# Performance work log

Hardware: AMD Instinct MI355X
Metric: run time of the kernel (lower is better)

The kernel has to match this reference:

```python
import jax, jax.numpy as jnp
import numpy as np

B, C, H, W = 4, 256, 64, 64
R, KH, KW = 4, 3, 3
K = KH * KW  # 9 kernel taps


def _conv2d(x, w, b):
    # plain 3x3 conv, stride 1, pad 1, NCHW
    y = jax.lax.conv_general_dilated(x, w, (1, 1), ((1, 1), (1, 1)),
                                     dimension_numbers=('NCHW', 'OIHW', 'NCHW'))
    return y + b[None, :, None, None]


def _bilinear_sample(x, py, px):
    # x: [B,C,H,W]; py,px: [B,K,H,W] float coords; zero padding outside the image.
    B_, C_, H_, W_ = x.shape
    xf = x.reshape(B_, C_, H_ * W_)
    y0 = jnp.floor(py)
    x0 = jnp.floor(px)
    wy = py - y0
    wx = px - x0
    y0i = y0.astype(jnp.int32)
    x0i = x0.astype(jnp.int32)

    def corner(yi, xi, wgt):
        valid = (yi >= 0) & (yi < H_) & (xi >= 0) & (xi < W_)
        idx = (jnp.clip(yi, 0, H_ - 1) * W_ + jnp.clip(xi, 0, W_ - 1)).reshape(B_, -1)
        vals = jax.vmap(lambda xb, ib: jnp.take(xb, ib, axis=1))(xf, idx)  # [B,C,K*H*W]
        vals = vals.reshape(B_, C_, K, H_, W_)
        w_ = (wgt * valid).astype(x.dtype)[:, None]  # [B,1,K,H,W]
        return vals * w_

    out = corner(y0i, x0i, (1 - wy) * (1 - wx))
    out = out + corner(y0i, x0i + 1, (1 - wy) * wx)
    out = out + corner(y0i + 1, x0i, wy * (1 - wx))
    out = out + corner(y0i + 1, x0i + 1, wy * wx)
    return out  # [B,C,K,H,W]


def _deform_conv(x, offset, weight):
    # DCNv1: offset [B, 2K, H, W], interleaved (dy, dx) per kernel tap.
    B_, C_, H_, W_ = x.shape
    off = offset.reshape(B_, K, 2, H_, W_)
    ky, kx = jnp.meshgrid(jnp.arange(KH), jnp.arange(KW), indexing='ij')
    base_y = (ky.reshape(K) - (KH - 1) // 2).astype(x.dtype)
    base_x = (kx.reshape(K) - (KW - 1) // 2).astype(x.dtype)
    py = (jnp.arange(H_, dtype=x.dtype)[None, None, :, None]
          + base_y[None, :, None, None] + off[:, :, 0])
    px = (jnp.arange(W_, dtype=x.dtype)[None, None, None, :]
          + base_x[None, :, None, None] + off[:, :, 1])
    sampled = _bilinear_sample(x, py, px)  # [B,C,K,H,W]
    wr = weight.reshape(weight.shape[0], C_, K)
    return jnp.einsum('bckhw,ock->bohw', sampled, wr)


def setup_inputs() -> dict:
    key = jax.random.key(0)
    k1, k2, k3 = jax.random.split(key, 3)
    x = jax.random.normal(k1, (B, C, H, W), jnp.float32)
    off_w = jax.random.normal(k2, (R, 2 * K, C, KH, KW), jnp.float32) * 0.01
    off_b = jnp.zeros((R, 2 * K), jnp.float32)
    w = jax.random.normal(k3, (R, C, C, KH, KW), jnp.float32) * (1.0 / np.sqrt(C * K))
    return {"x": x, "off_w": off_w, "off_b": off_b, "w": w}


def reference(x, off_w, off_b, w):
    for r in range(R):  # fixed small layer count
        offset = _conv2d(x, off_w[r], off_b[r])
        x = jax.nn.relu(_deform_conv(x, offset, w[r]))
    return x
```

## Files before the change

### kernel.cpp

```cpp
#include <hip/hip_runtime.h>


#define HW 4096

typedef __attribute__((ext_vector_type(8))) __bf16 bf16x8;
typedef __attribute__((ext_vector_type(4))) float f32x4;
typedef __attribute__((ext_vector_type(8))) unsigned short u16x8;

__device__ inline unsigned int f2bf_bits(float f) {
  unsigned int u = __float_as_uint(f);
  return (u + 0x7fffu + ((u >> 16) & 1u)) >> 16;
}
__device__ inline float bf_hi_f(unsigned short h) {
  return __uint_as_float(((unsigned int)h) << 16);
}

__global__ __launch_bounds__(256) void wpack_kernel(
    const float* __restrict__ w, unsigned short* __restrict__ wph) {
  const int f = blockIdx.x * 256 + threadIdx.x;
  const int j  = f & 7;
  const int l  = (f >> 3) & 63;
  const int nt = (f >> 9) & 15;
  const int q  = (f >> 13) % 72;
  const int r  = f / 589824;
  const int n  = nt * 16 + (l & 15);
  const int kk = q * 32 + ((l >> 4) << 3) + j;
  const int c  = kk & 255, k = kk >> 8;
  wph[f] = (unsigned short)f2bf_bits(w[((r * 256 + n) * 256 + c) * 9 + k]);
}

__global__ __launch_bounds__(256) void offwpack_kernel(
    const float* __restrict__ offw, unsigned short* __restrict__ owph) {
  const int f = blockIdx.x * 256 + threadIdx.x;
  const int j  = f & 7;
  const int l  = (f >> 3) & 63;
  const int nt = (f >> 9) & 1;
  const int q  = (f >> 10) % 72;
  const int r  = f / 73728;
  const int n  = nt * 16 + (l & 15);
  const int kk = q * 32 + ((l >> 4) << 3) + j;
  const int c  = kk & 255, k = kk >> 8;
  const float v = (n < 18) ? offw[((r * 18 + n) * 256 + c) * 9 + k] : 0.f;
  owph[f] = (unsigned short)f2bf_bits(v);
}

__global__ __launch_bounds__(256) void xpose_kernel(
    const float* __restrict__ x, unsigned short* __restrict__ xh) {
  const int p0 = blockIdx.x * 64;
  const int c0 = blockIdx.y * 64;
  const int b  = blockIdx.z;
  __shared__ float sT[64][65];
  const int t = threadIdx.x;
  const int pj = t & 63, ci0 = (t >> 6) * 16;
  const float* __restrict__ xb = x + ((size_t)(b * 256 + c0)) * HW + p0;
#pragma unroll
  for (int u = 0; u < 16; ++u)
    sT[ci0 + u][pj] = xb[(size_t)(ci0 + u) * HW + pj];
  __syncthreads();
  const int pr = t >> 2, cs = (t & 3) * 16;
  u16x8 va, vb;
#pragma unroll
  for (int u = 0; u < 8; ++u) va[u] = (unsigned short)f2bf_bits(sT[cs + u][pr]);
#pragma unroll
  for (int u = 0; u < 8; ++u) vb[u] = (unsigned short)f2bf_bits(sT[cs + 8 + u][pr]);
  const size_t o = ((size_t)b * HW + p0 + pr) * 256 + c0 + cs;
  *(u16x8*)(xh + o) = va;
  *(u16x8*)(xh + o + 8) = vb;
}

__global__ __launch_bounds__(256) void offconv_mfma(
    const unsigned short* __restrict__ xh,
    const unsigned short* __restrict__ owh,
    const float* __restrict__ bias, float* __restrict__ offs) {
  const int gid = blockIdx.x;
  const int b = (gid & 7) >> 1;
  const int idx = ((gid >> 3) << 1) | (gid & 1);
  const int h = idx >> 1, w0 = (idx & 1) << 5;
  const int t = threadIdx.x, lane = t & 63, wv = t >> 6;
  const int frow = lane & 15, fgrp = lane >> 4;
  const int mt = wv & 1, nt = wv >> 1;
  const int m = w0 + mt * 16 + frow;

  f32x4 acc = {0.f, 0.f, 0.f, 0.f};
  const u16x8 z8 = {};
  const size_t xb = (size_t)b * HW;

  for (int k = 0; k < 9; ++k) {
    const int ky = k / 3 - 1, kx = k % 3 - 1;
    if ((unsigned)(h + ky) >= 64u) continue;
    const bool vpx = (unsigned)(m + kx) < 64u;
    const int cpx = (m + kx) < 0 ? 0 : ((m + kx) > 63 ? 63 : (m + kx));
    const size_t abase = (xb + (size_t)((h + ky) * 64 + cpx)) * 256 + fgrp * 8;
#pragma unroll
    for (int cc = 0; cc < 8; ++cc) {
      const int q = k * 8 + cc;
      u16x8 ahr = *(const u16x8*)(xh + abase + cc * 32);
      if (!vpx) ahr = z8;
      const u16x8 bhr = ((const u16x8*)owh)[(q * 2 + nt) * 64 + lane];
      const bf16x8 ah = __builtin_bit_cast(bf16x8, ahr);
      const bf16x8 bh = __builtin_bit_cast(bf16x8, bhr);
      acc = __builtin_amdgcn_mfma_f32_16x16x32_bf16(ah, bh, acc, 0, 0, 0);
    }
  }
  const int oc = nt * 16 + frow;
  if (oc < 18) {
    const float bv = bias[oc];
    const int wbase = w0 + mt * 16 + fgrp * 4;
    float* __restrict__ op = offs + (size_t)(b * 18 + oc) * HW + h * 64 + wbase;
#pragma unroll
    for (int r = 0; r < 4; ++r) op[r] = acc[r] + bv;
  }
}

__global__ __launch_bounds__(512, 4) void deform_mfma(
    const unsigned short* __restrict__ xh,
    const float* __restrict__ offs,
    const unsigned short* __restrict__ wph,
    unsigned short* __restrict__ yth,
    float* __restrict__ outf) {
  const int gid = blockIdx.x;
  const int b = (gid & 7) >> 1;
  const int idx = ((gid >> 3) << 1) | (gid & 1);
  const int h = idx >> 1, w0 = (idx & 1) << 5;
  const int t = threadIdx.x, lane = t & 63, wv = t >> 6;
  const int frow = lane & 15, quad = lane >> 4;
  const int sm = t >> 4, cg = t & 15;

  __shared__ __align__(16) unsigned char smem[19456];
  float* s_cw = (float*)smem;
  int*   s_ci = (int*)(smem + 4608);
  unsigned char* sAb = smem + 9216;

  for (int i = t; i < 288; i += 512) {
    const int k = i >> 5, m = i & 31;
    const int ky = k / 3 - 1, kx = k % 3 - 1;
    const int mw = w0 + m;
    const int pos = h * 64 + mw;
    const float dy = offs[(b * 18 + 2 * k) * HW + pos];
    const float dx = offs[(b * 18 + 2 * k + 1) * HW + pos];
    const float py = (float)(h + ky) + dy;
    const float px = (float)(mw + kx) + dx;
    const float y0f = floorf(py), x0f = floorf(px);
    const float wy = py - y0f, wx = px - x0f;
    const int y0 = (int)y0f, x0 = (int)x0f;
#pragma unroll
    for (int j = 0; j < 4; ++j) {
      const int yi = y0 + (j >> 1), xi = x0 + (j & 1);
      const bool v = (yi >= 0) && (yi < 64) && (xi >= 0) && (xi < 64);
      const float wgt = ((j >> 1) ? wy : 1.f - wy) * ((j & 1) ? wx : 1.f - wx);
      s_cw[(k * 4 + j) * 32 + m] = v ? wgt : 0.f;
      const int yc = yi < 0 ? 0 : (yi > 63 ? 63 : yi);
      const int xc = xi < 0 ? 0 : (xi > 63 ? 63 : xi);
      s_ci[(k * 4 + j) * 32 + m] = yc * 64 + xc;
    }
  }
  __syncthreads();

  f32x4 acc[2][2];
#pragma unroll
  for (int mt = 0; mt < 2; ++mt)
#pragma unroll
    for (int nt = 0; nt < 2; ++nt) acc[mt][nt] = (f32x4){0.f, 0.f, 0.f, 0.f};

  const char* __restrict__ xbc = (const char*)(xh + (size_t)b * HW * 256);
  const u16x8* __restrict__ wp = (const u16x8*)wph;
  const int bfo = wv * 2;
  const int wbyte = sm * 80 + cg * 4;

  unsigned int G0[4], G1[4];
  u16x8 B0[2], B1[2];
  float cwr[4]; int cib[4];
#pragma unroll
  for (int j = 0; j < 4; ++j) {
    cwr[j] = s_cw[j * 32 + sm];
    cib[j] = s_ci[j * 32 + sm] * 512;
  }
#pragma unroll
  for (int j = 0; j < 4; ++j)
    G0[j] = *(const unsigned int*)(xbc + cib[j] + cg * 4);
#pragma unroll
  for (int i = 0; i < 2; ++i)
    B0[i] = wp[(bfo + i) * 64 + lane];

#define COMBINE_STORE(Gx, buf)                                              \
  {                                                                         \
    float s0 = cwr[0] * __uint_as_float(Gx[0] << 16);                       \
    float s1 = cwr[0] * __uint_as_float(Gx[0] & 0xffff0000u);               \
    s0 = fmaf(cwr[1], __uint_as_float(Gx[1] << 16), s0);                    \
    s1 = fmaf(cwr[1], __uint_as_float(Gx[1] & 0xffff0000u), s1);            \
    s0 = fmaf(cwr[2], __uint_as_float(Gx[2] << 16), s0);                    \
    s1 = fmaf(cwr[2], __uint_as_float(Gx[2] & 0xffff0000u), s1);            \
    s0 = fmaf(cwr[3], __uint_as_float(Gx[3] << 16), s0);                    \
    s1 = fmaf(cwr[3], __uint_as_float(Gx[3] & 0xffff0000u), s1);            \
    const unsigned int h0 = f2bf_bits(s0), h1 = f2bf_bits(s1);              \
    const unsigned int l0 = f2bf_bits(s0 - __uint_as_float(h0 << 16));      \
    const unsigned int l1 = f2bf_bits(s1 - __uint_as_float(h1 << 16));      \
    *(unsigned int*)(sAb + (buf) * 5120 + wbyte) = h0 | (h1 << 16);         \
    *(unsigned int*)(sAb + (buf) * 5120 + 2560 + wbyte) = l0 | (l1 << 16);  \
  }

#define MFMA_BODY(buf, Bx)                                                  \
  {                                                                         \
    bf16x8 ah[2], al[2];                                                    \
    _Pragma("unroll") for (int mt = 0; mt < 2; ++mt) {                      \
      const int rb = (mt * 16 + frow) * 80 + quad * 16;                     \
      ah[mt] = __builtin_bit_cast(                                          \
          bf16x8, *(const u16x8*)(sAb + (buf) * 5120 + rb));                \
      al[mt] = __builtin_bit_cast(                                          \
          bf16x8, *(const u16x8*)(sAb + (buf) * 5120 + 2560 + rb));         \
    }                                                                       \
    _Pragma("unroll") for (int nt = 0; nt < 2; ++nt) {                      \
      const bf16x8 bv = __builtin_bit_cast(bf16x8, Bx[nt]);                 \
      _Pragma("unroll") for (int mt = 0; mt < 2; ++mt) {                    \
        acc[mt][nt] = __builtin_amdgcn_mfma_f32_16x16x32_bf16(              \
            ah[mt], bv, acc[mt][nt], 0, 0, 0);                              \
        acc[mt][nt] = __builtin_amdgcn_mfma_f32_16x16x32_bf16(              \
            al[mt], bv, acc[mt][nt], 0, 0, 0);                              \
      }                                                                     \
    }                                                                       \
  }

  for (int it = 0; it < 36; ++it) {
    const int cc0 = it * 2;
    COMBINE_STORE(G0, 0)
    __syncthreads();
    {
      const int c0b = ((cc0 + 1) & 7) * 64 + cg * 4;
#pragma unroll
      for (int j = 0; j < 4; ++j)
        G1[j] = *(const unsigned int*)(xbc + cib[j] + c0b);
#pragma unroll
      for (int i = 0; i < 2; ++i)
        B1[i] = wp[((cc0 + 1) * 16 + bfo + i) * 64 + lane];
    }
    MFMA_BODY(0, B0)
    COMBINE_STORE(G1, 1)
    __syncthreads();
    if (it < 35) {
      const int cc2 = cc0 + 2;
      if ((cc2 & 7) == 0) {
        const int k = cc2 >> 3;
#pragma unroll
        for (int j = 0; j < 4; ++j) {
          cwr[j] = s_cw[(k * 4 + j) * 32 + sm];
          cib[j] = s_ci[(k * 4 + j) * 32 + sm] * 512;
        }
      }
      const int c0b = (cc2 & 7) * 64 + cg * 4;
#pragma unroll
      for (int j = 0; j < 4; ++j)
        G0[j] = *(const unsigned int*)(xbc + cib[j] + c0b);
#pragma unroll
      for (int i = 0; i < 2; ++i)
        B0[i] = wp[(cc2 * 16 + bfo + i) * 64 + lane];
    }
    MFMA_BODY(1, B1)
  }
#undef COMBINE_STORE
#undef MFMA_BODY

  if (outf) {
#pragma unroll
    for (int mt = 0; mt < 2; ++mt)
#pragma unroll
      for (int nt = 0; nt < 2; ++nt) {
        const int n = wv * 32 + nt * 16 + frow;
        const int pos = h * 64 + w0 + mt * 16 + quad * 4;
        float4 vv;
        vv.x = fmaxf(acc[mt][nt][0], 0.f);
        vv.y = fmaxf(acc[mt][nt][1], 0.f);
        vv.z = fmaxf(acc[mt][nt][2], 0.f);
        vv.w = fmaxf(acc[mt][nt][3], 0.f);
        *(float4*)&outf[(size_t)(b * 256 + n) * HW + pos] = vv;
      }
  } else {
    __syncthreads();
    unsigned short* sW = (unsigned short*)smem + wv * (32 * 36);
#pragma unroll
    for (int mt = 0; mt < 2; ++mt)
#pragma unroll
      for (int nt = 0; nt < 2; ++nt)
#pragma unroll
        for (int r = 0; r < 4; ++r)
          sW[(mt * 16 + quad * 4 + r) * 36 + nt * 16 + frow] =
              (unsigned short)f2bf_bits(fmaxf(acc[mt][nt][r], 0.f));
    __syncthreads();
    const int lm = lane & 31, cg2 = lane >> 5;
    const int pos = h * 64 + w0 + lm;
    unsigned short* __restrict__ yp =
        yth + ((size_t)b * HW + pos) * 256 + wv * 32 + cg2 * 16;
#pragma unroll
    for (int g = 0; g < 2; ++g)
      *(u16x8*)(yp + g * 8) = *(const u16x8*)&sW[lm * 36 + cg2 * 16 + g * 8];
  }
}

extern "C" void kernel_launch(void* const* d_in, const int* in_sizes, int n_in,
                              void* d_out, int out_size, void* d_ws, size_t ws_size,
                              hipStream_t stream) {
  const float* x0   = (const float*)d_in[0];
  const float* offw = (const float*)d_in[1];
  const float* offb = (const float*)d_in[2];
  const float* w    = (const float*)d_in[3];
  float* out = (float*)d_out;
  float* ws  = (float*)d_ws;

  float* offs = ws;
  unsigned short* wph  = (unsigned short*)(ws + 294912);
  unsigned short* owph = wph + 2359296;
  unsigned short* xTA  = owph + 294912;
  unsigned short* xTB  = xTA + 4194304;

  wpack_kernel<<<9216, 256, 0, stream>>>(w, wph);
  offwpack_kernel<<<1152, 256, 0, stream>>>(offw, owph);
  xpose_kernel<<<dim3(64, 4, 4), 256, 0, stream>>>(x0, xTA);

  unsigned short* pin = xTA;
  unsigned short* pout = xTB;
  for (int r = 0; r < 4; ++r) {
    offconv_mfma<<<512, 256, 0, stream>>>(pin, owph + r * 73728,
                                          offb + r * 18, offs);
    deform_mfma<<<512, 512, 0, stream>>>(pin, offs,
                                         wph + (size_t)r * 589824,
                                         (r < 3) ? pout : nullptr,
                                         (r < 3) ? nullptr : out);
    unsigned short* tmp = pin; pin = pout; pout = tmp;
  }
}
```

Before: 372.4 us.

## Split offset-conv K across waves, swizzle deform LDS, deepen gather prefetch

The offset conv now runs 8 waves per block and splits the channel-chunk loop in two, with an LDS reduction before the bias add and store. This adds parallelism to a low-occupancy kernel at the cost of a barrier and a small shared-memory reduction. The deform kernel replaces its padded 80-byte-stride LDS layout with an XOR-swizzled 128-byte-stride layout that interleaves the hi and lo bf16 halves, to cut bank conflicts and LDS usage. It also restructures the main loop by kernel tap so both gather buffers and weight fragments are prefetched one step further ahead, and the next tap's coordinates are loaded early.

```diff
diff --git a/kernel.cpp b/kernel.cpp
--- a/kernel.cpp
+++ b/kernel.cpp
@@ -68,7 +68,7 @@
   *(u16x8*)(xh + o + 8) = vb;
 }
 
-__global__ __launch_bounds__(256) void offconv_mfma(
+__global__ __launch_bounds__(512) void offconv_mfma(
     const unsigned short* __restrict__ xh,
     const unsigned short* __restrict__ owh,
     const float* __restrict__ bias, float* __restrict__ offs) {
@@ -78,7 +78,7 @@
   const int h = idx >> 1, w0 = (idx & 1) << 5;
   const int t = threadIdx.x, lane = t & 63, wv = t >> 6;
   const int frow = lane & 15, fgrp = lane >> 4;
-  const int mt = wv & 1, nt = wv >> 1;
+  const int mt = wv & 1, nt = (wv >> 1) & 1, kv = wv >> 2;
   const int m = w0 + mt * 16 + frow;
 
   f32x4 acc = {0.f, 0.f, 0.f, 0.f};
@@ -87,28 +87,39 @@
 
   for (int k = 0; k < 9; ++k) {
     const int ky = k / 3 - 1, kx = k % 3 - 1;
-    if ((unsigned)(h + ky) >= 64u) continue;
-    const bool vpx = (unsigned)(m + kx) < 64u;
-    const int cpx = (m + kx) < 0 ? 0 : ((m + kx) > 63 ? 63 : (m + kx));
-    const size_t abase = (xb + (size_t)((h + ky) * 64 + cpx)) * 256 + fgrp * 8;
-#pragma unroll
-    for (int cc = 0; cc < 8; ++cc) {
-      const int q = k * 8 + cc;
-      u16x8 ahr = *(const u16x8*)(xh + abase + cc * 32);
-      if (!vpx) ahr = z8;
-      const u16x8 bhr = ((const u16x8*)owh)[(q * 2 + nt) * 64 + lane];
-      const bf16x8 ah = __builtin_bit_cast(bf16x8, ahr);
-      const bf16x8 bh = __builtin_bit_cast(bf16x8, bhr);
-      acc = __builtin_amdgcn_mfma_f32_16x16x32_bf16(ah, bh, acc, 0, 0, 0);
+    if ((unsigned)(h + ky) < 64u) {
+      const bool vpx = (unsigned)(m + kx) < 64u;
+      const int cpx = (m + kx) < 0 ? 0 : ((m + kx) > 63 ? 63 : (m + kx));
+      const size_t abase = (xb + (size_t)((h + ky) * 64 + cpx)) * 256 + fgrp * 8;
+#pragma unroll
+      for (int j = 0; j < 4; ++j) {
+        const int cc = kv * 4 + j;
+        const int q = k * 8 + cc;
+        u16x8 ahr = *(const u16x8*)(xh + abase + cc * 32);
+        if (!vpx) ahr = z8;
+        const u16x8 bhr = ((const u16x8*)owh)[(q * 2 + nt) * 64 + lane];
+        const bf16x8 ah = __builtin_bit_cast(bf16x8, ahr);
+        const bf16x8 bh = __builtin_bit_cast(bf16x8, bhr);
+        acc = __builtin_amdgcn_mfma_f32_16x16x32_bf16(ah, bh, acc, 0, 0, 0);
+      }
     }
   }
-  const int oc = nt * 16 + frow;
-  if (oc < 18) {
-    const float bv = bias[oc];
-    const int wbase = w0 + mt * 16 + fgrp * 4;
-    float* __restrict__ op = offs + (size_t)(b * 18 + oc) * HW + h * 64 + wbase;
-#pragma unroll
-    for (int r = 0; r < 4; ++r) op[r] = acc[r] + bv;
+
+  __shared__ f32x4 red[2][2][64];
+  if (kv == 1) red[mt][nt][lane] = acc;
+  __syncthreads();
+  if (kv == 0) {
+    const f32x4 o = red[mt][nt][lane];
+    acc[0] += o[0]; acc[1] += o[1]; acc[2] += o[2]; acc[3] += o[3];
+    const int oc = nt * 16 + frow;
+    if (oc < 18) {
+      const float bv = bias[oc];
+      const int wbase = w0 + mt * 16 + fgrp * 4;
+      float* __restrict__ op =
+          offs + (size_t)(b * 18 + oc) * HW + h * 64 + wbase;
+#pragma unroll
+      for (int r = 0; r < 4; ++r) op[r] = acc[r] + bv;
+    }
   }
 }
 
@@ -126,7 +137,7 @@
   const int frow = lane & 15, quad = lane >> 4;
   const int sm = t >> 4, cg = t & 15;
 
-  __shared__ __align__(16) unsigned char smem[19456];
+  __shared__ __align__(16) unsigned char smem[18432];
   float* s_cw = (float*)smem;
   int*   s_ci = (int*)(smem + 4608);
   unsigned char* sAb = smem + 9216;
@@ -165,50 +176,62 @@
   const char* __restrict__ xbc = (const char*)(xh + (size_t)b * HW * 256);
   const u16x8* __restrict__ wp = (const u16x8*)wph;
   const int bfo = wv * 2;
-  const int wbyte = sm * 80 + cg * 4;
+
+  const int gs = ((sm & 3) << 1) | ((sm >> 2) & 1);
+  const int wbA = sm * 128 + ((((cg >> 2) ^ gs)) << 4) + (cg & 3) * 4;
+  const int wbL = wbA ^ 64;
+  const int gr = ((frow & 3) << 1) | ((frow >> 2) & 1);
+  const int rb0 = frow * 128 + ((quad ^ gr) << 4);
+  const int rb1 = rb0 + 2048;
 
   unsigned int G0[4], G1[4];
   u16x8 B0[2], B1[2];
-  float cwr[4]; int cib[4];
+  float cwrC[4], cwrN[4];
+  int cibC[4], cibN[4];
 #pragma unroll
   for (int j = 0; j < 4; ++j) {
-    cwr[j] = s_cw[j * 32 + sm];
-    cib[j] = s_ci[j * 32 + sm] * 512;
+    cwrC[j] = s_cw[j * 32 + sm];
+    cibC[j] = s_ci[j * 32 + sm] * 512;
   }
 #pragma unroll
   for (int j = 0; j < 4; ++j)
-    G0[j] = *(const unsigned int*)(xbc + cib[j] + cg * 4);
-#pragma unroll
-  for (int i = 0; i < 2; ++i)
-    B0[i] = wp[(bfo + i) * 64 + lane];
+    G0[j] = *(const unsigned int*)(xbc + cibC[j] + cg * 4);
+#pragma unroll
+  for (int j = 0; j < 4; ++j)
+    G1[j] = *(const unsigned int*)(xbc + cibC[j] + 64 + cg * 4);
+#pragma unroll
+  for (int i = 0; i < 2; ++i) B0[i] = wp[(bfo + i) * 64 + lane];
+#pragma unroll
+  for (int i = 0; i < 2; ++i) B1[i] = wp[(16 + bfo + i) * 64 + lane];
 
 #define COMBINE_STORE(Gx, buf)                                              \
   {                                                                         \
-    float s0 = cwr[0] * __uint_as_float(Gx[0] << 16);                       \
-    float s1 = cwr[0] * __uint_as_float(Gx[0] & 0xffff0000u);               \
-    s0 = fmaf(cwr[1], __uint_as_float(Gx[1] << 16), s0);                    \
-    s1 = fmaf(cwr[1], __uint_as_float(Gx[1] & 0xffff0000u), s1);            \
-    s0 = fmaf(cwr[2], __uint_as_float(Gx[2] << 16), s0);                    \
-    s1 = fmaf(cwr[2], __uint_as_float(Gx[2] & 0xffff0000u), s1);            \
-    s0 = fmaf(cwr[3], __uint_as_float(Gx[3] << 16), s0);                    \
-    s1 = fmaf(cwr[3], __uint_as_float(Gx[3] & 0xffff0000u), s1);            \
+    float s0 = cwrC[0] * __uint_as_float(Gx[0] << 16);                      \
+    float s1 = cwrC[0] * __uint_as_float(Gx[0] & 0xffff0000u);              \
+    s0 = fmaf(cwrC[1], __uint_as_float(Gx[1] << 16), s0);                   \
+    s1 = fmaf(cwrC[1], __uint_as_float(Gx[1] & 0xffff0000u), s1);           \
+    s0 = fmaf(cwrC[2], __uint_as_float(Gx[2] << 16), s0);                   \
+    s1 = fmaf(cwrC[2], __uint_as_float(Gx[2] & 0xffff0000u), s1);           \
+    s0 = fmaf(cwrC[3], __uint_as_float(Gx[3] << 16), s0);                   \
+    s1 = fmaf(cwrC[3], __uint_as_float(Gx[3] & 0xffff0000u), s1);           \
     const unsigned int h0 = f2bf_bits(s0), h1 = f2bf_bits(s1);              \
     const unsigned int l0 = f2bf_bits(s0 - __uint_as_float(h0 << 16));      \
     const unsigned int l1 = f2bf_bits(s1 - __uint_as_float(h1 << 16));      \
-    *(unsigned int*)(sAb + (buf) * 5120 + wbyte) = h0 | (h1 << 16);         \
-    *(unsigned int*)(sAb + (buf) * 5120 + 2560 + wbyte) = l0 | (l1 << 16);  \
+    *(unsigned int*)(sAb + (buf) * 4096 + wbA) = h0 | (h1 << 16);           \
+    *(unsigned int*)(sAb + (buf) * 4096 + wbL) = l0 | (l1 << 16);           \
   }
 
 #define MFMA_BODY(buf, Bx)                                                  \
   {                                                                         \
     bf16x8 ah[2], al[2];                                                    \
-    _Pragma("unroll") for (int mt = 0; mt < 2; ++mt) {                      \
-      const int rb = (mt * 16 + frow) * 80 + quad * 16;                     \
-      ah[mt] = __builtin_bit_cast(                                          \
-          bf16x8, *(const u16x8*)(sAb + (buf) * 5120 + rb));                \
-      al[mt] = __builtin_bit_cast(                                          \
-          bf16x8, *(const u16x8*)(sAb + (buf) * 5120 + 2560 + rb));         \
-    }                                                                       \
+    ah[0] = __builtin_bit_cast(                                             \
+        bf16x8, *(const u16x8*)(sAb + (buf) * 4096 + rb0));                 \
+    al[0] = __builtin_bit_cast(                                             \
+        bf16x8, *(const u16x8*)(sAb + (buf) * 4096 + (rb0 ^ 64)));          \
+    ah[1] = __builtin_bit_cast(                                             \
+        bf16x8, *(const u16x8*)(sAb + (buf) * 4096 + rb1));                 \
+    al[1] = __builtin_bit_cast(                                             \
+        bf16x8, *(const u16x8*)(sAb + (buf) * 4096 + (rb1 ^ 64)));          \
     _Pragma("unroll") for (int nt = 0; nt < 2; ++nt) {                      \
       const bf16x8 bv = __builtin_bit_cast(bf16x8, Bx[nt]);                 \
       _Pragma("unroll") for (int mt = 0; mt < 2; ++mt) {                    \
@@ -220,41 +243,62 @@
     }                                                                       \
   }
 
-  for (int it = 0; it < 36; ++it) {
-    const int cc0 = it * 2;
-    COMBINE_STORE(G0, 0)
-    __syncthreads();
-    {
-      const int c0b = ((cc0 + 1) & 7) * 64 + cg * 4;
-#pragma unroll
-      for (int j = 0; j < 4; ++j)
-        G1[j] = *(const unsigned int*)(xbc + cib[j] + c0b);
-#pragma unroll
-      for (int i = 0; i < 2; ++i)
-        B1[i] = wp[((cc0 + 1) * 16 + bfo + i) * 64 + lane];
+  for (int k9 = 0; k9 < 9; ++k9) {
+    const int cbase = k9 * 8;
+#pragma unroll
+    for (int j4 = 0; j4 < 4; ++j4) {
+      COMBINE_STORE(G0, 0)
+      __syncthreads();
+      if (k9 < 8 || j4 < 3) {
+        if (j4 == 3) {
+#pragma unroll
+          for (int j = 0; j < 4; ++j) {
+            cwrN[j] = s_cw[((k9 + 1) * 4 + j) * 32 + sm];
+            cibN[j] = s_ci[((k9 + 1) * 4 + j) * 32 + sm] * 512;
+          }
+#pragma unroll
+          for (int j = 0; j < 4; ++j)
+            G0[j] = *(const unsigned int*)(xbc + cibN[j] + cg * 4);
+        } else {
+          const int c0b = (2 * j4 + 2) * 64 + cg * 4;
+#pragma unroll
+          for (int j = 0; j < 4; ++j)
+            G0[j] = *(const unsigned int*)(xbc + cibC[j] + c0b);
+        }
+      }
+      MFMA_BODY(0, B0)
+      if (k9 < 8 || j4 < 3) {
+        const int c2 = cbase + 2 * j4 + 2;
+#pragma unroll
+        for (int i = 0; i < 2; ++i)
+          B0[i] = wp[(c2 * 16 + bfo + i) * 64 + lane];
+      }
+      COMBINE_STORE(G1, 1)
+      __syncthreads();
+      if (k9 < 8 || j4 < 3) {
+        if (j4 == 3) {
+#pragma unroll
+          for (int j = 0; j < 4; ++j)
+            G1[j] = *(const unsigned int*)(xbc + cibN[j] + 64 + cg * 4);
+        } else {
+          const int c1b = (2 * j4 + 3) * 64 + cg * 4;
+#pragma unroll
+          for (int j = 0; j < 4; ++j)
+            G1[j] = *(const unsigned int*)(xbc + cibC[j] + c1b);
+        }
+      }
+      MFMA_BODY(1, B1)
+      if (k9 < 8 || j4 < 3) {
+        const int c3 = cbase + 2 * j4 + 3;
+#pragma unroll
+        for (int i = 0; i < 2; ++i)
+          B1[i] = wp[(c3 * 16 + bfo + i) * 64 + lane];
+      }
+      if (j4 == 3 && k9 < 8) {
+#pragma unroll
+        for (int j = 0; j < 4; ++j) { cwrC[j] = cwrN[j]; cibC[j] = cibN[j]; }
+      }
     }
-    MFMA_BODY(0, B0)
-    COMBINE_STORE(G1, 1)
-    __syncthreads();
-    if (it < 35) {
-      const int cc2 = cc0 + 2;
-      if ((cc2 & 7) == 0) {
-        const int k = cc2 >> 3;
-#pragma unroll
-        for (int j = 0; j < 4; ++j) {
-          cwr[j] = s_cw[(k * 4 + j) * 32 + sm];
-          cib[j] = s_ci[(k * 4 + j) * 32 + sm] * 512;
-        }
-      }
-      const int c0b = (cc2 & 7) * 64 + cg * 4;
-#pragma unroll
-      for (int j = 0; j < 4; ++j)
-        G0[j] = *(const unsigned int*)(xbc + cib[j] + c0b);
-#pragma unroll
-      for (int i = 0; i < 2; ++i)
-        B0[i] = wp[(cc2 * 16 + bfo + i) * 64 + lane];
-    }
-    MFMA_BODY(1, B1)
   }
 #undef COMBINE_STORE
 #undef MFMA_BODY
@@ -318,7 +362,7 @@
   unsigned short* pin = xTA;
   unsigned short* pout = xTB;
   for (int r = 0; r < 4; ++r) {
-    offconv_mfma<<<512, 256, 0, stream>>>(pin, owph + r * 73728,
+    offconv_mfma<<<512, 512, 0, stream>>>(pin, owph + r * 73728,
                                           offb + r * 18, offs);
     deform_mfma<<<512, 512, 0, stream>>>(pin, offs,
                                          wph + (size_t)r * 589824,
```

Measured after the change: 363.6 us. 1.02x faster.
